# Optimization experiments

Measured on AMD Instinct MI355X. Metric: run time of the kernel, lower is better.

Reference implementation:

```python
import jax, jax.numpy as jnp
import numpy as np
from jax import lax
from jax.scipy.special import ndtri

T = 1 << 20  # time-series length
EPS = 1e-9
D_EPS = 1e-8
ALPHA = 0.99  # EMA decay for score variance


def setup_inputs() -> dict:
    key = jax.random.key(0)
    k1, k2 = jax.random.split(key)
    u = jax.random.uniform(k1, (T,), dtype=jnp.float32)
    v = jax.random.uniform(k2, (T,), dtype=jnp.float32)
    return {
        "u_data": u,
        "v_data": v,
        "omega": jnp.float32(0.0),
        "A": jnp.float32(0.05),
        "B_logit": jnp.float32(3.0),
    }


def reference(u_data, v_data, omega, A, B_logit):
    # rotation == 0 -> no rotation of (u, v)
    u = jnp.clip(u_data, EPS, 1.0 - EPS)
    v = jnp.clip(v_data, EPS, 1.0 - EPS)
    # precompute normal quantiles once (as torch code does with x_all/y_all)
    x = ndtri(u)
    y = ndtri(v)
    B = jax.nn.sigmoid(B_logit)

    def step(carry, xy):
        f, s_var = carry
        xt, yt = xy
        th = jnp.tanh(f)
        rho = 0.999 * th  # transform_parameter for gaussian family
        D = 1.0 - rho * rho + D_EPS
        sq = xt * xt + yt * yt
        z = sq - 2.0 * rho * xt * yt
        ll = -0.5 * jnp.log(D) - 0.5 * (z / D - sq)  # gaussian copula log-density
        # analytic score d ll / d f_t  (chain rule through rho = 0.999*tanh(f))
        dll_drho = rho / D + xt * yt / D - rho * z / (D * D)
        score = dll_drho * 0.999 * (1.0 - th * th)
        s_var_new = ALPHA * s_var + (1.0 - ALPHA) * score * score
        scaled = score / jnp.sqrt(s_var_new + 1e-8)
        f_new = omega + B * (f - omega) + A * scaled  # GAS(1,1) update
        return (f_new, s_var_new), ll

    init = (omega.astype(jnp.float32), jnp.float32(1.0))
    (_, _), lls = lax.scan(step, init, (x, y))
    return jnp.sum(lls)
```

## Files before the change

### kernel.cpp

```cpp
#include <hip/hip_runtime.h>
#include <hip/hip_bf16.h>


#define T_LEN     (1 << 20)
#define CHUNK_LEN 16
#define NCHUNK    (T_LEN / CHUNK_LEN)
#define WARM      256

__device__ __forceinline__ float ndtri_fast(float u) {
    float t = 2.0f * u - 1.0f;
    float w = -__logf(fmaxf(4.0f * u * (1.0f - u), 1e-38f));
    float p;
    if (w < 5.0f) {
        w = w - 2.5f;
        p =            2.81022636e-08f;
        p = fmaf(p, w, 3.43273939e-07f);
        p = fmaf(p, w, -3.5233877e-06f);
        p = fmaf(p, w, -4.39150654e-06f);
        p = fmaf(p, w, 0.00021858087f);
        p = fmaf(p, w, -0.00125372503f);
        p = fmaf(p, w, -0.00417768164f);
        p = fmaf(p, w, 0.246640727f);
        p = fmaf(p, w, 1.50140941f);
    } else {
        w = __builtin_amdgcn_sqrtf(w) - 3.0f;
        p =            -0.000200214257f;
        p = fmaf(p, w, 0.000100950558f);
        p = fmaf(p, w, 0.00134934322f);
        p = fmaf(p, w, -0.00367342844f);
        p = fmaf(p, w, 0.00573950773f);
        p = fmaf(p, w, -0.0076224613f);
        p = fmaf(p, w, 0.00943887047f);
        p = fmaf(p, w, 1.00167406f);
        p = fmaf(p, w, 2.83297682f);
    }
    return 1.41421356237f * p * t;
}

__global__ void prep_kernel(const float4* __restrict__ u4,
                            const float4* __restrict__ v4,
                            float4* __restrict__ sp4,
                            float* __restrict__ out) {
    int i = blockIdx.x * blockDim.x + threadIdx.x;
    if (i == 0) out[0] = 0.0f;
    float4 uu = u4[i];
    float4 vv = v4[i];
    float x0 = ndtri_fast(fminf(fmaxf(uu.x, 1e-9f), 1.0f - 1e-9f));
    float x1 = ndtri_fast(fminf(fmaxf(uu.y, 1e-9f), 1.0f - 1e-9f));
    float x2 = ndtri_fast(fminf(fmaxf(uu.z, 1e-9f), 1.0f - 1e-9f));
    float x3 = ndtri_fast(fminf(fmaxf(uu.w, 1e-9f), 1.0f - 1e-9f));
    float y0 = ndtri_fast(fminf(fmaxf(vv.x, 1e-9f), 1.0f - 1e-9f));
    float y1 = ndtri_fast(fminf(fmaxf(vv.y, 1e-9f), 1.0f - 1e-9f));
    float y2 = ndtri_fast(fminf(fmaxf(vv.z, 1e-9f), 1.0f - 1e-9f));
    float y3 = ndtri_fast(fminf(fmaxf(vv.w, 1e-9f), 1.0f - 1e-9f));
    float4 o0, o1;
    o0.x = fmaf(x0, x0, y0 * y0);  o0.y = -2.0f * x0 * y0;
    o0.z = fmaf(x1, x1, y1 * y1);  o0.w = -2.0f * x1 * y1;
    o1.x = fmaf(x2, x2, y2 * y2);  o1.y = -2.0f * x2 * y2;
    o1.z = fmaf(x3, x3, y3 * y3);  o1.w = -2.0f * x3 * y3;
    sp4[2 * i]     = o0;
    sp4[2 * i + 1] = o1;
}

template <bool LL>
__device__ __forceinline__ float gas_step(float sq, float m2p,
                                          float& f, float& s,
                                          float omega, float A, float B) {
    float E    = __expf(2.0f * f);
    float r    = __builtin_amdgcn_rcpf(E + 1.0f);
    float rho  = fmaf(-1.998f, r, 0.999f);
    float gg   = 3.996f * r * (1.0f - r);
    float D    = fmaf(-rho, rho, 1.0f);
    float invD = __builtin_amdgcn_rcpf(D);
    float z    = fmaf(rho, m2p, sq);
    float zi   = z * invD;
    float ll   = 0.0f;
    if (LL) ll = fmaf(-0.5f, __logf(D), 0.5f * (sq - zi));
    float pxy  = -0.5f * m2p;
    float dll  = fmaf(-rho, zi, rho + pxy) * invD;
    float score  = dll * gg;
    float snew   = fmaf(0.99f, s, 0.01f * (score * score));
    float scaled = score * __builtin_amdgcn_rsqf(snew + 1e-8f);
    f = fmaf(A, scaled, fmaf(B, f - omega, omega));
    s = snew;
    return ll;
}

__launch_bounds__(256, 1)
__global__ void scan_kernel(const float2* __restrict__ sp,
                            const float* __restrict__ p_omega,
                            const float* __restrict__ p_A,
                            const float* __restrict__ p_Blogit,
                            float* __restrict__ out) {
    const int c = blockIdx.x * blockDim.x + threadIdx.x;
    const float omega = p_omega[0];
    const float A     = p_A[0];
    const float B     = 1.0f / (1.0f + __expf(-p_Blogit[0]));

    const int t0     = c * CHUNK_LEN - WARM;
    const int tstart = (t0 < 0) ? 0 : t0;
    const int warm   = (t0 < 0) ? (c * CHUNK_LEN) : WARM;
    const int Gw     = warm >> 2;

    const float4* __restrict__ pf = (const float4*)(sp + tstart);

    float4 l0 = pf[2 * Gw + 0], l1 = pf[2 * Gw + 1];
    float4 l2 = pf[2 * Gw + 2], l3 = pf[2 * Gw + 3];
    float4 l4 = pf[2 * Gw + 4], l5 = pf[2 * Gw + 5];
    float4 l6 = pf[2 * Gw + 6], l7 = pf[2 * Gw + 7];

    float f = omega, s = 1.0f;

    if (Gw > 0) {
        float4 a = pf[0], b = pf[1];
        for (int g = 0; g < Gw; ++g) {
            int gn = (g + 1 < Gw) ? (g + 1) : g;
            float4 na = pf[2 * gn];
            float4 nb = pf[2 * gn + 1];
            gas_step<false>(a.x, a.y, f, s, omega, A, B);
            gas_step<false>(a.z, a.w, f, s, omega, A, B);
            gas_step<false>(b.x, b.y, f, s, omega, A, B);
            gas_step<false>(b.z, b.w, f, s, omega, A, B);
            a = na; b = nb;
        }
    }

    float acc;
    acc  = gas_step<true>(l0.x, l0.y, f, s, omega, A, B);
    acc += gas_step<true>(l0.z, l0.w, f, s, omega, A, B);
    acc += gas_step<true>(l1.x, l1.y, f, s, omega, A, B);
    acc += gas_step<true>(l1.z, l1.w, f, s, omega, A, B);
    acc += gas_step<true>(l2.x, l2.y, f, s, omega, A, B);
    acc += gas_step<true>(l2.z, l2.w, f, s, omega, A, B);
    acc += gas_step<true>(l3.x, l3.y, f, s, omega, A, B);
    acc += gas_step<true>(l3.z, l3.w, f, s, omega, A, B);
    acc += gas_step<true>(l4.x, l4.y, f, s, omega, A, B);
    acc += gas_step<true>(l4.z, l4.w, f, s, omega, A, B);
    acc += gas_step<true>(l5.x, l5.y, f, s, omega, A, B);
    acc += gas_step<true>(l5.z, l5.w, f, s, omega, A, B);
    acc += gas_step<true>(l6.x, l6.y, f, s, omega, A, B);
    acc += gas_step<true>(l6.z, l6.w, f, s, omega, A, B);
    acc += gas_step<true>(l7.x, l7.y, f, s, omega, A, B);
    acc += gas_step<true>(l7.z, l7.w, f, s, omega, A, B);

    __shared__ float red[256];
    red[threadIdx.x] = acc;
    __syncthreads();
    for (int off = 128; off > 0; off >>= 1) {
        if (threadIdx.x < off) red[threadIdx.x] += red[threadIdx.x + off];
        __syncthreads();
    }
    if (threadIdx.x == 0) atomicAdd(out, red[0]);
}

extern "C" void kernel_launch(void* const* d_in, const int* in_sizes, int n_in,
                              void* d_out, int out_size, void* d_ws, size_t ws_size,
                              hipStream_t stream) {
    const float* u       = (const float*)d_in[0];
    const float* v       = (const float*)d_in[1];
    const float* omega   = (const float*)d_in[2];
    const float* A       = (const float*)d_in[3];
    const float* B_logit = (const float*)d_in[4];
    float*       out     = (float*)d_out;
    float2*      sp      = (float2*)d_ws;

    prep_kernel<<<T_LEN / 4 / 256, 256, 0, stream>>>(
        (const float4*)u, (const float4*)v, (float4*)sp, out);
    scan_kernel<<<NCHUNK / 256, 256, 0, stream>>>(sp, omega, A, B_logit, out);
}
```

Measured before the change: 96.19 us.

## Fuse ndtri prep into scan kernel and rescale GAS state to exp2 domain

Removes the separate prep kernel and its workspace round-trip, so the scan kernel reads u and v directly and computes the normal quantiles inline, pipelined one group ahead of the recurrence. Because of the warm-up overlap, each chunk recomputes ndtri for its 256 warm-up samples, which roughly multiplies the transcendental work by 17. The recurrence state is rescaled so that tanh uses exp2 directly, and the score algebra is rearranged to shorten the serial dependency chain. Zeroing the output moves to a memset.

```diff
diff --git a/kernel.cpp b/kernel.cpp
--- a/kernel.cpp
+++ b/kernel.cpp
@@ -1,11 +1,16 @@
 #include <hip/hip_runtime.h>
-#include <hip/hip_bf16.h>
 
 
 #define T_LEN     (1 << 20)
 #define CHUNK_LEN 16
 #define NCHUNK    (T_LEN / CHUNK_LEN)
 #define WARM      256
+
+#if __has_builtin(__builtin_amdgcn_exp2f)
+#define EXP2F(x) __builtin_amdgcn_exp2f(x)
+#else
+#define EXP2F(x) __expf(0.69314718056f * (x))
+#endif
 
 __device__ __forceinline__ float ndtri_fast(float u) {
     float t = 2.0f * u - 1.0f;
@@ -37,57 +42,51 @@
     return 1.41421356237f * p * t;
 }
 
-__global__ void prep_kernel(const float4* __restrict__ u4,
-                            const float4* __restrict__ v4,
-                            float4* __restrict__ sp4,
-                            float* __restrict__ out) {
-    int i = blockIdx.x * blockDim.x + threadIdx.x;
-    if (i == 0) out[0] = 0.0f;
-    float4 uu = u4[i];
-    float4 vv = v4[i];
-    float x0 = ndtri_fast(fminf(fmaxf(uu.x, 1e-9f), 1.0f - 1e-9f));
-    float x1 = ndtri_fast(fminf(fmaxf(uu.y, 1e-9f), 1.0f - 1e-9f));
-    float x2 = ndtri_fast(fminf(fmaxf(uu.z, 1e-9f), 1.0f - 1e-9f));
-    float x3 = ndtri_fast(fminf(fmaxf(uu.w, 1e-9f), 1.0f - 1e-9f));
-    float y0 = ndtri_fast(fminf(fmaxf(vv.x, 1e-9f), 1.0f - 1e-9f));
-    float y1 = ndtri_fast(fminf(fmaxf(vv.y, 1e-9f), 1.0f - 1e-9f));
-    float y2 = ndtri_fast(fminf(fmaxf(vv.z, 1e-9f), 1.0f - 1e-9f));
-    float y3 = ndtri_fast(fminf(fmaxf(vv.w, 1e-9f), 1.0f - 1e-9f));
-    float4 o0, o1;
-    o0.x = fmaf(x0, x0, y0 * y0);  o0.y = -2.0f * x0 * y0;
-    o0.z = fmaf(x1, x1, y1 * y1);  o0.w = -2.0f * x1 * y1;
-    o1.x = fmaf(x2, x2, y2 * y2);  o1.y = -2.0f * x2 * y2;
-    o1.z = fmaf(x3, x3, y3 * y3);  o1.w = -2.0f * x3 * y3;
-    sp4[2 * i]     = o0;
-    sp4[2 * i + 1] = o1;
+__device__ __forceinline__ void cop_pair(float uu, float vv,
+                                         float& sq, float& xy) {
+    float x = ndtri_fast(fminf(fmaxf(uu, 1e-9f), 1.0f - 1e-9f));
+    float y = ndtri_fast(fminf(fmaxf(vv, 1e-9f), 1.0f - 1e-9f));
+    sq = fmaf(x, x, y * y);
+    xy = x * y;
 }
 
 template <bool LL>
-__device__ __forceinline__ float gas_step(float sq, float m2p,
-                                          float& f, float& s,
-                                          float omega, float A, float B) {
-    float E    = __expf(2.0f * f);
+__device__ __forceinline__ float gas_stepF(float sq, float xy,
+                                           float& F, float& s,
+                                           float OmegaF, float AK, float B) {
+    float E    = EXP2F(F);
     float r    = __builtin_amdgcn_rcpf(E + 1.0f);
     float rho  = fmaf(-1.998f, r, 0.999f);
+    float n2r  = fmaf(3.996f, r, -1.998f);
     float gg   = 3.996f * r * (1.0f - r);
     float D    = fmaf(-rho, rho, 1.0f);
     float invD = __builtin_amdgcn_rcpf(D);
-    float z    = fmaf(rho, m2p, sq);
-    float zi   = z * invD;
-    float ll   = 0.0f;
-    if (LL) ll = fmaf(-0.5f, __logf(D), 0.5f * (sq - zi));
-    float pxy  = -0.5f * m2p;
-    float dll  = fmaf(-rho, zi, rho + pxy) * invD;
-    float score  = dll * gg;
-    float snew   = fmaf(0.99f, s, 0.01f * (score * score));
-    float scaled = score * __builtin_amdgcn_rsqf(snew + 1e-8f);
-    f = fmaf(A, scaled, fmaf(B, f - omega, omega));
-    s = snew;
-    return ll;
+    float z    = fmaf(n2r, xy, sq);
+    float rxyD = (rho + xy) * D;
+    float N    = fmaf(-rho, z, rxyD);
+    float invD2 = invD * invD;
+    float dll  = N * invD2;
+    float base = fmaf(B, F - OmegaF, OmegaF);
+    float cpre = fmaf(0.99f, s, 1e-8f);
+    float s99  = 0.99f * s;
+    float g01  = gg * 0.1f;
+    float gA   = gg * AK;
+    float sc01 = dll * g01;
+    float scA  = dll * gA;
+    float t    = fmaf(sc01, sc01, cpre);
+    float inv  = __builtin_amdgcn_rsqf(t);
+    s          = fmaf(sc01, sc01, s99);
+    F          = fmaf(scA, inv, base);
+    if (LL) {
+        float zi = z * invD;
+        return fmaf(-0.5f, __logf(D), 0.5f * (sq - zi));
+    }
+    return 0.0f;
 }
 
 __launch_bounds__(256, 1)
-__global__ void scan_kernel(const float2* __restrict__ sp,
+__global__ void scan_kernel(const float4* __restrict__ u4,
+                            const float4* __restrict__ v4,
                             const float* __restrict__ p_omega,
                             const float* __restrict__ p_A,
                             const float* __restrict__ p_Blogit,
@@ -96,52 +95,74 @@
     const float omega = p_omega[0];
     const float A     = p_A[0];
     const float B     = 1.0f / (1.0f + __expf(-p_Blogit[0]));
+    const float KAP   = 2.8853900817779268f;
+    const float OmegaF = omega * KAP;
+    const float AK     = A * KAP;
 
     const int t0     = c * CHUNK_LEN - WARM;
     const int tstart = (t0 < 0) ? 0 : t0;
     const int warm   = (t0 < 0) ? (c * CHUNK_LEN) : WARM;
     const int Gw     = warm >> 2;
 
-    const float4* __restrict__ pf = (const float4*)(sp + tstart);
+    const float4* __restrict__ pu = u4 + (tstart >> 2);
+    const float4* __restrict__ pv = v4 + (tstart >> 2);
 
-    float4 l0 = pf[2 * Gw + 0], l1 = pf[2 * Gw + 1];
-    float4 l2 = pf[2 * Gw + 2], l3 = pf[2 * Gw + 3];
-    float4 l4 = pf[2 * Gw + 4], l5 = pf[2 * Gw + 5];
-    float4 l6 = pf[2 * Gw + 6], l7 = pf[2 * Gw + 7];
+    float4 lu0 = pu[Gw + 0], lv0 = pv[Gw + 0];
+    float4 lu1 = pu[Gw + 1], lv1 = pv[Gw + 1];
+    float4 lu2 = pu[Gw + 2], lv2 = pv[Gw + 2];
+    float4 lu3 = pu[Gw + 3], lv3 = pv[Gw + 3];
 
-    float f = omega, s = 1.0f;
+    float lsq[16], lxy[16];
+    cop_pair(lu0.x, lv0.x, lsq[0],  lxy[0]);
+    cop_pair(lu0.y, lv0.y, lsq[1],  lxy[1]);
+    cop_pair(lu0.z, lv0.z, lsq[2],  lxy[2]);
+    cop_pair(lu0.w, lv0.w, lsq[3],  lxy[3]);
+    cop_pair(lu1.x, lv1.x, lsq[4],  lxy[4]);
+    cop_pair(lu1.y, lv1.y, lsq[5],  lxy[5]);
+    cop_pair(lu1.z, lv1.z, lsq[6],  lxy[6]);
+    cop_pair(lu1.w, lv1.w, lsq[7],  lxy[7]);
+    cop_pair(lu2.x, lv2.x, lsq[8],  lxy[8]);
+    cop_pair(lu2.y, lv2.y, lsq[9],  lxy[9]);
+    cop_pair(lu2.z, lv2.z, lsq[10], lxy[10]);
+    cop_pair(lu2.w, lv2.w, lsq[11], lxy[11]);
+    cop_pair(lu3.x, lv3.x, lsq[12], lxy[12]);
+    cop_pair(lu3.y, lv3.y, lsq[13], lxy[13]);
+    cop_pair(lu3.z, lv3.z, lsq[14], lxy[14]);
+    cop_pair(lu3.w, lv3.w, lsq[15], lxy[15]);
+
+    float F = OmegaF, s = 1.0f;
 
     if (Gw > 0) {
-        float4 a = pf[0], b = pf[1];
+        float4 cu = pu[0], cv = pv[0];
+        int g1 = (Gw > 1) ? 1 : 0;
+        float4 nu = pu[g1], nv = pv[g1];
+        float csq0, cxy0, csq1, cxy1, csq2, cxy2, csq3, cxy3;
+        cop_pair(cu.x, cv.x, csq0, cxy0);
+        cop_pair(cu.y, cv.y, csq1, cxy1);
+        cop_pair(cu.z, cv.z, csq2, cxy2);
+        cop_pair(cu.w, cv.w, csq3, cxy3);
         for (int g = 0; g < Gw; ++g) {
-            int gn = (g + 1 < Gw) ? (g + 1) : g;
-            float4 na = pf[2 * gn];
-            float4 nb = pf[2 * gn + 1];
-            gas_step<false>(a.x, a.y, f, s, omega, A, B);
-            gas_step<false>(a.z, a.w, f, s, omega, A, B);
-            gas_step<false>(b.x, b.y, f, s, omega, A, B);
-            gas_step<false>(b.z, b.w, f, s, omega, A, B);
-            a = na; b = nb;
+            int gf = g + 2; gf = (gf < Gw) ? gf : (Gw - 1);
+            float4 fu = pu[gf], fv = pv[gf];
+            float nsq0, nxy0, nsq1, nxy1, nsq2, nxy2, nsq3, nxy3;
+            cop_pair(nu.x, nv.x, nsq0, nxy0);
+            cop_pair(nu.y, nv.y, nsq1, nxy1);
+            cop_pair(nu.z, nv.z, nsq2, nxy2);
+            cop_pair(nu.w, nv.w, nsq3, nxy3);
+            gas_stepF<false>(csq0, cxy0, F, s, OmegaF, AK, B);
+            gas_stepF<false>(csq1, cxy1, F, s, OmegaF, AK, B);
+            gas_stepF<false>(csq2, cxy2, F, s, OmegaF, AK, B);
+            gas_stepF<false>(csq3, cxy3, F, s, OmegaF, AK, B);
+            csq0 = nsq0; cxy0 = nxy0; csq1 = nsq1; cxy1 = nxy1;
+            csq2 = nsq2; cxy2 = nxy2; csq3 = nsq3; cxy3 = nxy3;
+            nu = fu; nv = fv;
         }
     }
 
-    float acc;
-    acc  = gas_step<true>(l0.x, l0.y, f, s, omega, A, B);
-    acc += gas_step<true>(l0.z, l0.w, f, s, omega, A, B);
-    acc += gas_step<true>(l1.x, l1.y, f, s, omega, A, B);
-    acc += gas_step<true>(l1.z, l1.w, f, s, omega, A, B);
-    acc += gas_step<true>(l2.x, l2.y, f, s, omega, A, B);
-    acc += gas_step<true>(l2.z, l2.w, f, s, omega, A, B);
-    acc += gas_step<true>(l3.x, l3.y, f, s, omega, A, B);
-    acc += gas_step<true>(l3.z, l3.w, f, s, omega, A, B);
-    acc += gas_step<true>(l4.x, l4.y, f, s, omega, A, B);
-    acc += gas_step<true>(l4.z, l4.w, f, s, omega, A, B);
-    acc += gas_step<true>(l5.x, l5.y, f, s, omega, A, B);
-    acc += gas_step<true>(l5.z, l5.w, f, s, omega, A, B);
-    acc += gas_step<true>(l6.x, l6.y, f, s, omega, A, B);
-    acc += gas_step<true>(l6.z, l6.w, f, s, omega, A, B);
-    acc += gas_step<true>(l7.x, l7.y, f, s, omega, A, B);
-    acc += gas_step<true>(l7.z, l7.w, f, s, omega, A, B);
+    float acc = 0.0f;
+#pragma unroll
+    for (int i = 0; i < 16; ++i)
+        acc += gas_stepF<true>(lsq[i], lxy[i], F, s, OmegaF, AK, B);
 
     __shared__ float red[256];
     red[threadIdx.x] = acc;
@@ -156,15 +177,16 @@
 extern "C" void kernel_launch(void* const* d_in, const int* in_sizes, int n_in,
                               void* d_out, int out_size, void* d_ws, size_t ws_size,
                               hipStream_t stream) {
+    (void)in_sizes; (void)n_in; (void)out_size; (void)d_ws; (void)ws_size;
     const float* u       = (const float*)d_in[0];
     const float* v       = (const float*)d_in[1];
     const float* omega   = (const float*)d_in[2];
     const float* A       = (const float*)d_in[3];
     const float* B_logit = (const float*)d_in[4];
     float*       out     = (float*)d_out;
-    float2*      sp      = (float2*)d_ws;
 
-    prep_kernel<<<T_LEN / 4 / 256, 256, 0, stream>>>(
-        (const float4*)u, (const float4*)v, (float4*)sp, out);
-    scan_kernel<<<NCHUNK / 256, 256, 0, stream>>>(sp, omega, A, B_logit, out);
+    hipMemsetAsync(out, 0, sizeof(float), stream);
+
+    scan_kernel<<<NCHUNK / 256, 256, 0, stream>>>(
+        (const float4*)u, (const float4*)v, omega, A, B_logit, out);
 }
```

After: 141.8 us. 47.4% more time.

## Reformulate GAS step to remove transcendentals via Newton-tracked reciprocals

Applied to the files above, without the earlier changes.

Rewrites the per-step GAS recurrence in a rescaled state (F = f times 2/ln2), so exp becomes a native exp2 and rho, D and the score come out as rational functions of E. The per-step rcp and rsqrt on the serial dependency chain are replaced by Newton-Raphson refinement of reciprocals carried over from the previous step, with a wave-wide fallback to hardware rcp when the estimate drifts. The inverse square root of the variance is tracked multiplicatively via a one-step Newton update. This trades extra FMAs and a divergence check for a shorter critical-path latency per step, and it risks accuracy drift in the tracked reciprocal and rsqrt estimates.

```diff
diff --git a/kernel.cpp b/kernel.cpp
--- a/kernel.cpp
+++ b/kernel.cpp
@@ -1,11 +1,16 @@
 #include <hip/hip_runtime.h>
-#include <hip/hip_bf16.h>
 
 
 #define T_LEN     (1 << 20)
 #define CHUNK_LEN 16
 #define NCHUNK    (T_LEN / CHUNK_LEN)
 #define WARM      256
+
+#if __has_builtin(__builtin_amdgcn_exp2f)
+#define EXP2F(x) __builtin_amdgcn_exp2f(x)
+#else
+#define EXP2F(x) __expf(0.69314718056f * (x))
+#endif
 
 __device__ __forceinline__ float ndtri_fast(float u) {
     float t = 2.0f * u - 1.0f;
@@ -64,26 +69,69 @@
 
 template <bool LL>
 __device__ __forceinline__ float gas_step(float sq, float m2p,
-                                          float& f, float& s,
-                                          float omega, float A, float B) {
-    float E    = __expf(2.0f * f);
-    float r    = __builtin_amdgcn_rcpf(E + 1.0f);
-    float rho  = fmaf(-1.998f, r, 0.999f);
-    float gg   = 3.996f * r * (1.0f - r);
-    float D    = fmaf(-rho, rho, 1.0f);
-    float invD = __builtin_amdgcn_rcpf(D);
+                                          float& F, float& s, float& sig,
+                                          float& nh2, float& cs,
+                                          float& invQ, float& invR,
+                                          float OmegaF, float B, float cAK) {
+    float E   = EXP2F(F);
+    float P   = E + 1.0f;
+    float Mm  = E - 1.0f;
+    float a_  = fmaf(-0.999f, Mm, P);
+    float b_  = fmaf( 0.999f, Mm, P);
+    float Q   = a_ * b_;
+    float R   = P * P;
+    float kMP = 0.999f * (Mm * P);
+
+    float eR = R * invR;
+    float eQ = Q * invQ;
+    if (__any(fabsf(eR - 1.0f) > 0.35f || fabsf(eQ - 1.0f) > 0.35f)) {
+        invR = __builtin_amdgcn_rcpf(R);
+        invQ = __builtin_amdgcn_rcpf(Q);
+        eR = R * invR;
+        eQ = Q * invQ;
+    }
+    float txR = invR + invR;
+    float x1R = fmaf(-eR, invR, txR);
+    float e2R = R * x1R;
+    float tx2R = x1R + x1R;
+    invR = fmaf(-e2R, x1R, tx2R);
+    float txQ = invQ + invQ;
+    float x1Q = fmaf(-eQ, invQ, txQ);
+    float e2Q = Q * x1Q;
+    float tx2Q = x1Q + x1Q;
+    invQ = fmaf(-e2Q, x1Q, tx2Q);
+
+    float rho  = kMP * invR;
     float z    = fmaf(rho, m2p, sq);
-    float zi   = z * invD;
-    float ll   = 0.0f;
-    if (LL) ll = fmaf(-0.5f, __logf(D), 0.5f * (sq - zi));
-    float pxy  = -0.5f * m2p;
-    float dll  = fmaf(-rho, zi, rho + pxy) * invD;
-    float score  = dll * gg;
-    float snew   = fmaf(0.99f, s, 0.01f * (score * score));
-    float scaled = score * __builtin_amdgcn_rsqf(snew + 1e-8f);
-    f = fmaf(A, scaled, fmaf(B, f - omega, omega));
-    s = snew;
-    return ll;
+    float rpxy = fmaf(-0.5f, m2p, rho);
+    float iQ2  = invQ * invQ;
+    float t1   = rpxy * invQ;
+    float zk   = z * kMP;
+    float t2   = zk * iQ2;
+    float inner = t1 - t2;
+
+    float pe   = 0.3996f * E;
+    float scg  = pe * inner;
+    float c1   = cs * E;
+    float scAp = c1 * inner;
+    float cpre = fmaf(0.99f, s, 1e-8f);
+    float s99  = 0.99f * s;
+    float t    = fmaf(scg, scg, cpre);
+    float w    = fmaf(nh2, t, 1.5f);
+    float base = fmaf(B, F - OmegaF, OmegaF);
+    F = fmaf(scAp, w, base);
+
+    s   = fmaf(scg, scg, s99);
+    sig = sig * w;
+    nh2 = -0.5f * (sig * sig);
+    cs  = cAK * sig;
+
+    if (LL) {
+        float Dv  = Q * invR;
+        float ziv = z * (R * invQ);
+        return fmaf(-0.5f, __logf(Dv), 0.5f * (sq - ziv));
+    }
+    return 0.0f;
 }
 
 __launch_bounds__(256, 1)
@@ -96,6 +144,9 @@
     const float omega = p_omega[0];
     const float A     = p_A[0];
     const float B     = 1.0f / (1.0f + __expf(-p_Blogit[0]));
+    const float KAP   = 2.8853900817779268f;
+    const float OmegaF = omega * KAP;
+    const float cAK    = A * KAP * 3.996f;
 
     const int t0     = c * CHUNK_LEN - WARM;
     const int tstart = (t0 < 0) ? 0 : t0;
@@ -109,7 +160,14 @@
     float4 l4 = pf[2 * Gw + 4], l5 = pf[2 * Gw + 5];
     float4 l6 = pf[2 * Gw + 6], l7 = pf[2 * Gw + 7];
 
-    float f = omega, s = 1.0f;
+    float F = OmegaF, s = 1.0f;
+    float sig = 1.0f, nh2 = -0.5f, cs = cAK;
+    float E0 = EXP2F(F);
+    float P0 = E0 + 1.0f, M0 = E0 - 1.0f;
+    float R0 = P0 * P0;
+    float Q0 = fmaf(-0.999f, M0, P0) * fmaf(0.999f, M0, P0);
+    float invR = __builtin_amdgcn_rcpf(R0);
+    float invQ = __builtin_amdgcn_rcpf(Q0);
 
     if (Gw > 0) {
         float4 a = pf[0], b = pf[1];
@@ -117,31 +175,31 @@
             int gn = (g + 1 < Gw) ? (g + 1) : g;
             float4 na = pf[2 * gn];
             float4 nb = pf[2 * gn + 1];
-            gas_step<false>(a.x, a.y, f, s, omega, A, B);
-            gas_step<false>(a.z, a.w, f, s, omega, A, B);
-            gas_step<false>(b.x, b.y, f, s, omega, A, B);
-            gas_step<false>(b.z, b.w, f, s, omega, A, B);
+            gas_step<false>(a.x, a.y, F, s, sig, nh2, cs, invQ, invR, OmegaF, B, cAK);
+            gas_step<false>(a.z, a.w, F, s, sig, nh2, cs, invQ, invR, OmegaF, B, cAK);
+            gas_step<false>(b.x, b.y, F, s, sig, nh2, cs, invQ, invR, OmegaF, B, cAK);
+            gas_step<false>(b.z, b.w, F, s, sig, nh2, cs, invQ, invR, OmegaF, B, cAK);
             a = na; b = nb;
         }
     }
 
     float acc;
-    acc  = gas_step<true>(l0.x, l0.y, f, s, omega, A, B);
-    acc += gas_step<true>(l0.z, l0.w, f, s, omega, A, B);
-    acc += gas_step<true>(l1.x, l1.y, f, s, omega, A, B);
-    acc += gas_step<true>(l1.z, l1.w, f, s, omega, A, B);
-    acc += gas_step<true>(l2.x, l2.y, f, s, omega, A, B);
-    acc += gas_step<true>(l2.z, l2.w, f, s, omega, A, B);
-    acc += gas_step<true>(l3.x, l3.y, f, s, omega, A, B);
-    acc += gas_step<true>(l3.z, l3.w, f, s, omega, A, B);
-    acc += gas_step<true>(l4.x, l4.y, f, s, omega, A, B);
-    acc += gas_step<true>(l4.z, l4.w, f, s, omega, A, B);
-    acc += gas_step<true>(l5.x, l5.y, f, s, omega, A, B);
-    acc += gas_step<true>(l5.z, l5.w, f, s, omega, A, B);
-    acc += gas_step<true>(l6.x, l6.y, f, s, omega, A, B);
-    acc += gas_step<true>(l6.z, l6.w, f, s, omega, A, B);
-    acc += gas_step<true>(l7.x, l7.y, f, s, omega, A, B);
-    acc += gas_step<true>(l7.z, l7.w, f, s, omega, A, B);
+    acc  = gas_step<true>(l0.x, l0.y, F, s, sig, nh2, cs, invQ, invR, OmegaF, B, cAK);
+    acc += gas_step<true>(l0.z, l0.w, F, s, sig, nh2, cs, invQ, invR, OmegaF, B, cAK);
+    acc += gas_step<true>(l1.x, l1.y, F, s, sig, nh2, cs, invQ, invR, OmegaF, B, cAK);
+    acc += gas_step<true>(l1.z, l1.w, F, s, sig, nh2, cs, invQ, invR, OmegaF, B, cAK);
+    acc += gas_step<true>(l2.x, l2.y, F, s, sig, nh2, cs, invQ, invR, OmegaF, B, cAK);
+    acc += gas_step<true>(l2.z, l2.w, F, s, sig, nh2, cs, invQ, invR, OmegaF, B, cAK);
+    acc += gas_step<true>(l3.x, l3.y, F, s, sig, nh2, cs, invQ, invR, OmegaF, B, cAK);
+    acc += gas_step<true>(l3.z, l3.w, F, s, sig, nh2, cs, invQ, invR, OmegaF, B, cAK);
+    acc += gas_step<true>(l4.x, l4.y, F, s, sig, nh2, cs, invQ, invR, OmegaF, B, cAK);
+    acc += gas_step<true>(l4.z, l4.w, F, s, sig, nh2, cs, invQ, invR, OmegaF, B, cAK);
+    acc += gas_step<true>(l5.x, l5.y, F, s, sig, nh2, cs, invQ, invR, OmegaF, B, cAK);
+    acc += gas_step<true>(l5.z, l5.w, F, s, sig, nh2, cs, invQ, invR, OmegaF, B, cAK);
+    acc += gas_step<true>(l6.x, l6.y, F, s, sig, nh2, cs, invQ, invR, OmegaF, B, cAK);
+    acc += gas_step<true>(l6.z, l6.w, F, s, sig, nh2, cs, invQ, invR, OmegaF, B, cAK);
+    acc += gas_step<true>(l7.x, l7.y, F, s, sig, nh2, cs, invQ, invR, OmegaF, B, cAK);
+    acc += gas_step<true>(l7.z, l7.w, F, s, sig, nh2, cs, invQ, invR, OmegaF, B, cAK);
 
     __shared__ float red[256];
     red[threadIdx.x] = acc;
@@ -156,6 +214,7 @@
 extern "C" void kernel_launch(void* const* d_in, const int* in_sizes, int n_in,
                               void* d_out, int out_size, void* d_ws, size_t ws_size,
                               hipStream_t stream) {
+    (void)in_sizes; (void)n_in; (void)out_size; (void)ws_size;
     const float* u       = (const float*)d_in[0];
     const float* v       = (const float*)d_in[1];
     const float* omega   = (const float*)d_in[2];
```

Measured after the change: 106.6 us. 1.11x slower.
